# Performance work log

Measured on AMD Instinct MI355X. Metric: run time of the kernel, lower is better.

## Reference

```python
import jax, jax.numpy as jnp
import numpy as np

B, L, D = 4, 2048, 1024
H, DK, DV = 16, 64, 64


def setup_inputs() -> dict:
    key = jax.random.key(0)
    ks = jax.random.split(key, 11)
    s = 1.0 / np.sqrt(D)
    so = 1.0 / np.sqrt(H * DV)
    return {
        "query": jax.random.normal(ks[0], (B, L, D), jnp.float32),
        "key": jax.random.normal(ks[1], (B, L, D), jnp.float32),
        "value": jax.random.normal(ks[2], (B, L, D), jnp.float32),
        "W_q": jax.random.uniform(ks[3], (D, H * DK), jnp.float32, -s, s),
        "b_q": jax.random.uniform(ks[4], (H * DK,), jnp.float32, -s, s),
        "W_k": jax.random.uniform(ks[5], (D, H * DK), jnp.float32, -s, s),
        "b_k": jax.random.uniform(ks[6], (H * DK,), jnp.float32, -s, s),
        "W_v": jax.random.uniform(ks[7], (D, H * DV), jnp.float32, -s, s),
        "b_v": jax.random.uniform(ks[8], (H * DV,), jnp.float32, -s, s),
        "W_o": jax.random.uniform(ks[9], (H * DV, D), jnp.float32, -so, so),
        "b_o": jax.random.uniform(ks[10], (D,), jnp.float32, -so, so),
    }


def reference(query, key, value, W_q, b_q, W_k, b_k, W_v, b_v, W_o, b_o):
    # QKV projections, then split heads: [B, L, H*d] -> [B, H, L, d]
    q = (query @ W_q + b_q).reshape(B, L, H, DK).transpose(0, 2, 1, 3)
    k = (key @ W_k + b_k).reshape(B, L, H, DK).transpose(0, 2, 1, 3)
    v = (value @ W_v + b_v).reshape(B, L, H, DV).transpose(0, 2, 1, 3)
    # scaled dot-product attention: softmax(q k^T / sqrt(dk)) v
    scores = jnp.einsum("bhqd,bhkd->bhqk", q, k) / jnp.sqrt(jnp.float32(DK))
    attn = jax.nn.softmax(scores, axis=-1)
    ctx = jnp.einsum("bhqk,bhkd->bhqd", attn, v)
    # combine heads: [B, H, L, dv] -> [B, L, H*dv], output projection
    out = ctx.transpose(0, 2, 1, 3).reshape(B, L, H * DV) @ W_o + b_o
    return out
```

## Files before the change

kernel.cpp:

```cpp
#include <hip/hip_runtime.h>

#define BATCH 4
#define LSEQ 2048
#define DMODEL 1024
#define NHEAD 16
#define DHEAD 64
#define MTOT (BATCH * LSEQ)

typedef _Float16 f16;
typedef _Float16 f16x8 __attribute__((ext_vector_type(8)));
typedef _Float16 f16x4 __attribute__((ext_vector_type(4)));
typedef __fp16 h16x2 __attribute__((ext_vector_type(2)));
typedef float f32x4 __attribute__((ext_vector_type(4)));
typedef float f32x16 __attribute__((ext_vector_type(16)));
typedef unsigned int u32;
typedef unsigned int u32x4 __attribute__((ext_vector_type(4)));

#define SCORE_SCALE 0.180336878f

typedef const __attribute__((address_space(1))) void gvoid;
typedef __attribute__((address_space(3))) void lvoid;
#define GLDS16(g, l) __builtin_amdgcn_global_load_lds((gvoid*)(g), (lvoid*)(l), 16, 0, 0)

#define WAITCNT(s) do { asm volatile("s_waitcnt " s ::: "memory"); \
                        __builtin_amdgcn_sched_barrier(0); } while (0)
#define BAR() __builtin_amdgcn_s_barrier()
#define SCHED0() __builtin_amdgcn_sched_barrier(0)

__global__ __launch_bounds__(256)
void prep(const float* __restrict__ in0, const float* __restrict__ in1,
          const float* __restrict__ in2, f16* __restrict__ out, int n8,
          const float* __restrict__ W0, const float* __restrict__ W1,
          const float* __restrict__ W2, const float* __restrict__ W3,
          f16* __restrict__ WtBase)
{
    __shared__ float T[64][68];
    const int t = threadIdx.x;
    const int y = blockIdx.y;

    if (y < 3) {
        const float* in = (y == 0) ? in0 : (y == 1) ? in1 : in2;
        f16* o = out + (size_t)y * (size_t)n8 * 8;
        int i = blockIdx.x * 256 + t;
        if (i >= n8) return;
        float4 a = ((const float4*)in)[2 * i];
        float4 b = ((const float4*)in)[2 * i + 1];
        f16x8 v;
        v[0] = (f16)a.x; v[1] = (f16)a.y; v[2] = (f16)a.z; v[3] = (f16)a.w;
        v[4] = (f16)b.x; v[5] = (f16)b.y; v[6] = (f16)b.z; v[7] = (f16)b.w;
        ((f16x8*)o)[i] = v;
        return;
    }

    const int id = blockIdx.x;
    if (id >= 1024) return;
    const int z = id >> 8, rem = id & 255;
    const int k0 = (rem >> 4) * 64, n0 = (rem & 15) * 64;
    const float* W = (z == 0) ? W0 : (z == 1) ? W1 : (z == 2) ? W2 : W3;
    f16* Wt = WtBase + (size_t)z * DMODEL * DMODEL;
    const int tr = t >> 4, tc = (t & 15) * 4;
#pragma unroll
    for (int p = 0; p < 64; p += 16) {
        float4 v = *(const float4*)&W[(size_t)(k0 + tr + p) * DMODEL + n0 + tc];
        *(float4*)&T[tr + p][tc] = v;
    }
    __syncthreads();
    const int n = t >> 2, kc = (t & 3) * 16;
    f16x8 o0, o1;
#pragma unroll
    for (int j = 0; j < 8; ++j) o0[j] = (f16)T[kc + j][n];
#pragma unroll
    for (int j = 0; j < 8; ++j) o1[j] = (f16)T[kc + 8 + j][n];
    *(f16x8*)&Wt[(size_t)(n0 + n) * DMODEL + k0 + kc] = o0;
    *(f16x8*)&Wt[(size_t)(n0 + n) * DMODEL + k0 + kc + 8] = o1;
}

__global__ __launch_bounds__(512, 2)
void gemm_qkv(const f16* __restrict__ A, const f16* __restrict__ Bt,
              const float* __restrict__ b0, const float* __restrict__ b1,
              const float* __restrict__ b2, f16* __restrict__ Cout)
{
    __shared__ f16 As[2][2][128][64];
    __shared__ f16 Bs[2][2][128][64];

    const int t = threadIdx.x;
    const int lane = t & 63;
    const int w = t >> 6, wr = w >> 2, wc = w & 3;
    const int quad = lane >> 4, m16 = lane & 15;
    const int m0 = blockIdx.x * 256, n0 = blockIdx.y * 256;
    const int which = n0 >> 10;

    const int sr = t >> 3;
    const int sc = ((t & 7) << 4) ^ ((sr & 7) << 4);
    const f16* Asrc = A + (size_t)which * MTOT * DMODEL
                        + (size_t)(m0 + sr) * DMODEL + (sc >> 1);
    const f16* Bsrc = Bt + (size_t)(n0 + sr) * DMODEL + (sc >> 1);

    auto stA = [&](int buf, int h, int kt) {
        const f16* s = Asrc + (size_t)(h * 128) * DMODEL + kt * 64;
        GLDS16(s,               &As[buf][h][0][0] + t * 8);
        GLDS16(s + 64 * DMODEL, &As[buf][h][64][0] + t * 8);
    };
    auto stB = [&](int buf, int h, int kt) {
        const f16* s = Bsrc + (size_t)(h * 128) * DMODEL + kt * 64;
        GLDS16(s,               &Bs[buf][h][0][0] + t * 8);
        GLDS16(s + 64 * DMODEL, &Bs[buf][h][64][0] + t * 8);
    };
    auto stageTile = [&](int k) {
        const int b = k & 1;
        stA(b, 0, k); stA(b, 1, k); stB(b, 0, k); stB(b, 1, k);
    };

    const int fsw = (m16 & 7) << 4;
    auto rdA = [&](int buf, int mf, int ks) -> f16x8 {
        return *(const f16x8*)((const char*)&As[buf][wr][0][0]
                               + (mf * 16 + m16) * 128
                               + ((ks * 64 + quad * 16) ^ fsw));
    };
    auto rdB = [&](int buf, int nf, int ks) -> f16x8 {
        return *(const f16x8*)((const char*)&Bs[buf][wc >> 1][0][0]
                               + ((wc & 1) * 64 + nf * 16 + m16) * 128
                               + ((ks * 64 + quad * 16) ^ fsw));
    };

    f32x4 acc[8][4] = {};

    auto compute = [&](int buf) {
        f16x8 af[4][2], bf[4][2];
#pragma unroll
        for (int nf = 0; nf < 4; ++nf)
#pragma unroll
            for (int ks = 0; ks < 2; ++ks)
                bf[nf][ks] = rdB(buf, nf, ks);
#pragma unroll
        for (int mg = 0; mg < 2; ++mg) {
#pragma unroll
            for (int mi = 0; mi < 4; ++mi)
#pragma unroll
                for (int ks = 0; ks < 2; ++ks)
                    af[mi][ks] = rdA(buf, mg * 4 + mi, ks);
#pragma unroll
            for (int mi = 0; mi < 4; ++mi)
#pragma unroll
                for (int ni = 0; ni < 4; ++ni)
#pragma unroll
                    for (int ks = 0; ks < 2; ++ks)
                        acc[mg * 4 + mi][ni] =
                            __builtin_amdgcn_mfma_f32_16x16x32_f16(
                                af[mi][ks], bf[ni][ks],
                                acc[mg * 4 + mi][ni], 0, 0, 0);
        }
    };

    const int NKT = DMODEL / 64;
    stageTile(0);
    stageTile(1);

#pragma unroll 2
    for (int k = 0; k < NKT - 2; ++k) {
        WAITCNT("vmcnt(8)");
        BAR(); SCHED0();
        compute(k & 1);
        WAITCNT("lgkmcnt(0)");
        BAR(); SCHED0();
        stageTile(k + 2);
        SCHED0();
    }
    WAITCNT("vmcnt(8)");
    BAR(); SCHED0();
    compute((NKT - 2) & 1);
    WAITCNT("lgkmcnt(0)");
    BAR(); SCHED0();
    WAITCNT("vmcnt(0)");
    BAR(); SCHED0();
    compute((NKT - 1) & 1);

    const float* bp = (which == 0) ? b0 : (which == 1) ? b1 : b2;
    const float scale = (which == 0) ? SCORE_SCALE : 1.0f;
    f16* o = Cout + (size_t)which * MTOT * DMODEL;
    float bv[4];
    int hh[4], dd[4];
#pragma unroll
    for (int nf = 0; nf < 4; ++nf) {
        const int nn = (n0 + wc * 64 + nf * 16 + m16) & 1023;
        bv[nf] = bp[nn];
        hh[nf] = nn >> 6;
        dd[nf] = nn & 63;
    }
#pragma unroll
    for (int mf = 0; mf < 8; ++mf) {
        const int mrow = m0 + wr * 128 + mf * 16 + quad * 4;
        const int b = mrow >> 11, l0 = mrow & (LSEQ - 1);
        if (which < 2) {
#pragma unroll
            for (int j = 0; j < 4; ++j)
#pragma unroll
                for (int nf = 0; nf < 4; ++nf) {
                    const float v = (acc[mf][nf][j] + bv[nf]) * scale;
                    o[(((size_t)(b * NHEAD + hh[nf]) * LSEQ + l0 + j) << 6)
                      + dd[nf]] = (f16)v;
                }
        } else {
#pragma unroll
            for (int nf = 0; nf < 4; ++nf) {
                f16x4 pk;
#pragma unroll
                for (int j = 0; j < 4; ++j) pk[j] = (f16)(acc[mf][nf][j] + bv[nf]);
                *(f16x4*)&o[(((size_t)(b * NHEAD + hh[nf]) << 6) + dd[nf]) * LSEQ
                            + l0] = pk;
            }
        }
    }
}

__global__ __launch_bounds__(256)
void gemm_f16(const f16* __restrict__ A, const f16* __restrict__ Bt,
              const float* __restrict__ b0, void* __restrict__ Cout)
{
    __shared__ f16 As2[2][128][32];
    __shared__ f16 Bs2[2][128][32];

    const int t = threadIdx.x;
    const int lane = t & 63, w = t >> 6;
    const int quad = lane >> 4, m16 = lane & 15;
    const int m0 = blockIdx.x * 128;
    const int n0 = blockIdx.y * 128;
    const int wm = (w & 1) * 64, wn = (w >> 1) * 64;

    f32x4 acc[4][4] = {};

    const f16* Ag = A + (size_t)(m0 + (t >> 2)) * DMODEL + (t & 3) * 8;
    const f16* Bg = Bt + (size_t)(n0 + (t >> 2)) * DMODEL + (t & 3) * 8;
    f16* Al = &As2[0][0][0] + t * 8;
    f16* Bl = &Bs2[0][0][0] + t * 8;

    for (int k0 = 0; k0 < DMODEL; k0 += 64) {
        __syncthreads();
#pragma unroll
        for (int h = 0; h < 2; ++h) {
            GLDS16(Ag + k0 + h * 32, Al + h * 4096);
            GLDS16(Ag + k0 + h * 32 + (size_t)64 * DMODEL, Al + h * 4096 + 2048);
            GLDS16(Bg + k0 + h * 32, Bl + h * 4096);
            GLDS16(Bg + k0 + h * 32 + (size_t)64 * DMODEL, Bl + h * 4096 + 2048);
        }
        __syncthreads();
#pragma unroll
        for (int h = 0; h < 2; ++h) {
            f16x8 af[4], bf[4];
#pragma unroll
            for (int mi = 0; mi < 4; ++mi)
                af[mi] = *(const f16x8*)&As2[h][wm + mi * 16 + m16][quad * 8];
#pragma unroll
            for (int ni = 0; ni < 4; ++ni)
                bf[ni] = *(const f16x8*)&Bs2[h][wn + ni * 16 + m16][quad * 8];
#pragma unroll
            for (int mi = 0; mi < 4; ++mi)
#pragma unroll
                for (int ni = 0; ni < 4; ++ni)
                    acc[mi][ni] = __builtin_amdgcn_mfma_f32_16x16x32_f16(
                        af[mi], bf[ni], acc[mi][ni], 0, 0, 0);
        }
    }

#pragma unroll
    for (int ni = 0; ni < 4; ++ni) {
        const int n = n0 + wn + ni * 16 + m16;
        const float bv = b0[n];
#pragma unroll
        for (int mi = 0; mi < 4; ++mi)
#pragma unroll
            for (int j = 0; j < 4; ++j) {
                const int m = m0 + wm + mi * 16 + quad * 4 + j;
                ((float*)Cout)[(size_t)m * DMODEL + n] = acc[mi][ni][j] + bv;
            }
    }
}

__global__ __launch_bounds__(256, 4)
void attn_mfma(const f16* __restrict__ Qh, const f16* __restrict__ Kh,
               const f16* __restrict__ Vt, f16* __restrict__ ctx)
{
    __shared__ f16 Ks[2][64 * 64];
    __shared__ f16 Vs[2][64 * 64];

    const int t = threadIdx.x;
    const int lane = t & 63, w = t >> 6;
    const int l31 = lane & 31;
    const int hi = lane >> 5;
    const int swz = (l31 & 7) << 4;

    const int bid = blockIdx.x;
    const int x = bid & 7, rest = bid >> 3;
    const int qt = rest & 15;
    const int g = x + 8 * (rest >> 4);
    const int q0 = qt * 128 + w * 32;

    const f16* Qg = Qh + (size_t)g * LSEQ * DHEAD;
    const f16* Kg = Kh + (size_t)g * LSEQ * DHEAD;
    const f16* Vg = Vt + (size_t)g * LSEQ * DHEAD;

    f16x8 qf[4];
#pragma unroll
    for (int s = 0; s < 4; ++s)
        qf[s] = *(const f16x8*)&Qg[(size_t)(q0 + l31) * DHEAD + 16 * s + 8 * hi];

    const int srow = t >> 3;
    const int sxs = ((t & 7) << 4) ^ ((srow & 7) << 4);
    const f16* ksrcA = Kg + (size_t)srow * DHEAD + (sxs >> 1);
    const f16* vsrcA = Vg + (size_t)srow * LSEQ + (sxs >> 1);
    const f16* ksrcB = ksrcA + (size_t)32 * DHEAD;
    const f16* vsrcB = vsrcA + (size_t)32 * LSEQ;
    f16* kd[2] = {&Ks[0][0] + t * 8, &Ks[1][0] + t * 8};
    f16* vd[2] = {&Vs[0][0] + t * 8, &Vs[1][0] + t * 8};

    auto stage = [&](int b, int kt) {
        GLDS16(ksrcA + (size_t)kt * DHEAD, kd[b]);
        GLDS16(ksrcB + (size_t)kt * DHEAD, kd[b] + 2048);
        GLDS16(vsrcA + kt, vd[b]);
        GLDS16(vsrcB + kt, vd[b] + 2048);
    };

    f32x16 ctxa[2] = {};
    float lsum = 0.f;

    stage(0, 0);
    __syncthreads();

    auto proc = [&](const f32x16& stv, const int kb, const char* Vc) {
        u32 d[8];
        const h16x2 one2 = {(__fp16)1.0f, (__fp16)1.0f};
#pragma unroll
        for (int r = 0; r < 8; ++r) {
            const float p0 = __builtin_amdgcn_exp2f(stv[2 * r]);
            const float p1 = __builtin_amdgcn_exp2f(stv[2 * r + 1]);
            const h16x2 pk = __builtin_amdgcn_cvt_pkrtz(p0, p1);
#if __has_builtin(__builtin_amdgcn_fdot2)
            lsum = __builtin_amdgcn_fdot2(pk, one2, lsum, false);
#else
            lsum += p0 + p1;
#endif
            d[r] = __builtin_bit_cast(u32, pk);
        }
#pragma unroll
        for (int s = 0; s < 2; ++s) {
            const u32 sendE = hi ? d[4 * s + 0] : d[4 * s + 2];
            const u32 sendO = hi ? d[4 * s + 1] : d[4 * s + 3];
            const u32 recvE = __shfl_xor(sendE, 32);
            const u32 recvO = __shfl_xor(sendO, 32);
            u32x4 paw;
            paw[0] = hi ? recvE : d[4 * s + 0];
            paw[1] = hi ? recvO : d[4 * s + 1];
            paw[2] = hi ? d[4 * s + 2] : recvE;
            paw[3] = hi ? d[4 * s + 3] : recvO;
            const f16x8 pa = __builtin_bit_cast(f16x8, paw);
            const int kbyte = kb * 64 + 32 * s + 16 * hi;
#pragma unroll
            for (int d32 = 0; d32 < 2; ++d32) {
                const int vrow = d32 * 32 + l31;
                const f16x8 vf = *(const f16x8*)(Vc + vrow * 128 + (kbyte ^ swz));
                ctxa[d32] = __builtin_amdgcn_mfma_f32_32x32x16_f16(
                    pa, vf, ctxa[d32], 0, 0, 0);
            }
        }
    };

    auto compute = [&](const f16* Kbuf, const f16* Vbuf) {
        const char* Kc = (const char*)Kbuf;
        const char* Vc = (const char*)Vbuf;
        f32x16 s0 = {}, s1 = {};
#pragma unroll
        for (int s = 0; s < 4; ++s) {
            const int cb = 32 * s + 16 * hi;
            const f16x8 kf0 = *(const f16x8*)(Kc + l31 * 128 + (cb ^ swz));
            const f16x8 kf1 = *(const f16x8*)(Kc + (l31 + 32) * 128 + (cb ^ swz));
            s0 = __builtin_amdgcn_mfma_f32_32x32x16_f16(kf0, qf[s], s0, 0, 0, 0);
            s1 = __builtin_amdgcn_mfma_f32_32x32x16_f16(kf1, qf[s], s1, 0, 0, 0);
        }
        proc(s0, 0, Vc);
        proc(s1, 1, Vc);
    };

    for (int kt = 0; kt < LSEQ; kt += 128) {
        if (kt + 64 < LSEQ) stage(1, kt + 64);
        compute(&Ks[0][0], &Vs[0][0]);
        __syncthreads();
        if (kt + 128 < LSEQ) stage(0, kt + 128);
        compute(&Ks[1][0], &Vs[1][0]);
        __syncthreads();
    }

    const float l = lsum + __shfl_xor(lsum, 32);
    const float linv = 1.0f / l;
    const int batch = g >> 4, h = g & 15;
#pragma unroll
    for (int r = 0; r < 16; ++r) {
        const int qr = (r & 3) + 8 * (r >> 2) + 4 * hi;
        const float inv = __shfl(linv, qr);
        f16* op = ctx + ((size_t)(batch * LSEQ + q0 + qr)) * DMODEL
                      + h * 64 + l31;
        op[0]  = (f16)(ctxa[0][r] * inv);
        op[32] = (f16)(ctxa[1][r] * inv);
    }
}

extern "C" void kernel_launch(void* const* d_in, const int* in_sizes, int n_in,
                              void* d_out, int out_size, void* d_ws, size_t ws_size,
                              hipStream_t stream)
{
    const float* query = (const float*)d_in[0];
    const float* key   = (const float*)d_in[1];
    const float* value = (const float*)d_in[2];
    const float* W_q   = (const float*)d_in[3];
    const float* b_q   = (const float*)d_in[4];
    const float* W_k   = (const float*)d_in[5];
    const float* b_k   = (const float*)d_in[6];
    const float* W_v   = (const float*)d_in[7];
    const float* b_v   = (const float*)d_in[8];
    const float* W_o   = (const float*)d_in[9];
    const float* b_o   = (const float*)d_in[10];
    float* out = (float*)d_out;

    const size_t MAT = (size_t)MTOT * DMODEL;
    f16* base = (f16*)d_ws;
    f16* Aq   = base;
    f16* Qhp  = base + 3 * MAT;
    f16* ctxh = base + 6 * MAT;
    f16* Wtq  = base + 7 * MAT;
    f16* Wto  = Wtq + (size_t)3 * DMODEL * DMODEL;

    const int n8 = (int)(MAT / 8);
    prep<<<dim3(n8 / 256, 4), 256, 0, stream>>>(
        query, key, value, Aq, n8, W_q, W_k, W_v, W_o, Wtq);

    gemm_qkv<<<dim3(MTOT / 256, 3 * DMODEL / 256), 512, 0, stream>>>(
        Aq, Wtq, b_q, b_k, b_v, Qhp);

    attn_mfma<<<BATCH * NHEAD * (LSEQ / 128), 256, 0, stream>>>(
        Qhp, Qhp + MAT, Qhp + 2 * MAT, ctxh);

    gemm_f16<<<dim3(MTOT / 128, DMODEL / 128), 256, 0, stream>>>(
        ctxh, Wto, b_o, out);
}
```

Measured before the change: 342.0 us.

## Split attention KV tiles across wave pairs with 1024-thread blocks and LDS reduction

The attention kernel now runs 1024-thread blocks covering 256 query rows. Each pair of waves splits every 128-key tile between them, one taking the even half and one the odd half. The partial context sums and softmax denominators are then combined through shared memory. K/V staging moves to larger 128-key tiles with a wider V swizzle and explicit waitcnt/barrier pipelining, which amortizes K/V loads over more query rows. The trade-offs are an extra LDS reduction and larger blocks that may limit occupancy.

```diff
diff --git a/kernel.cpp b/kernel.cpp
--- a/kernel.cpp
+++ b/kernel.cpp
@@ -276,24 +276,26 @@
     }
 }
 
-__global__ __launch_bounds__(256, 4)
+__global__ __launch_bounds__(1024, 8)
 void attn_mfma(const f16* __restrict__ Qh, const f16* __restrict__ Kh,
                const f16* __restrict__ Vt, f16* __restrict__ ctx)
 {
-    __shared__ f16 Ks[2][64 * 64];
-    __shared__ f16 Vs[2][64 * 64];
+    __shared__ float SMf[16896];
+    char* smem = (char*)SMf;
 
     const int t = threadIdx.x;
     const int lane = t & 63, w = t >> 6;
+    const int qsub = w >> 1, par = w & 1;
     const int l31 = lane & 31;
     const int hi = lane >> 5;
-    const int swz = (l31 & 7) << 4;
+    const int swzK = (l31 & 7) << 4;
+    const int swzV = (l31 & 15) << 4;
 
     const int bid = blockIdx.x;
     const int x = bid & 7, rest = bid >> 3;
-    const int qt = rest & 15;
-    const int g = x + 8 * (rest >> 4);
-    const int q0 = qt * 128 + w * 32;
+    const int qt = rest & 7;
+    const int g = x + 8 * (rest >> 3);
+    const int q0 = qt * 256 + qsub * 32;
 
     const f16* Qg = Qh + (size_t)g * LSEQ * DHEAD;
     const f16* Kg = Kh + (size_t)g * LSEQ * DHEAD;
@@ -304,27 +306,20 @@
     for (int s = 0; s < 4; ++s)
         qf[s] = *(const f16x8*)&Qg[(size_t)(q0 + l31) * DHEAD + 16 * s + 8 * hi];
 
-    const int srow = t >> 3;
-    const int sxs = ((t & 7) << 4) ^ ((srow & 7) << 4);
-    const f16* ksrcA = Kg + (size_t)srow * DHEAD + (sxs >> 1);
-    const f16* vsrcA = Vg + (size_t)srow * LSEQ + (sxs >> 1);
-    const f16* ksrcB = ksrcA + (size_t)32 * DHEAD;
-    const f16* vsrcB = vsrcA + (size_t)32 * LSEQ;
-    f16* kd[2] = {&Ks[0][0] + t * 8, &Ks[1][0] + t * 8};
-    f16* vd[2] = {&Vs[0][0] + t * 8, &Vs[1][0] + t * 8};
-
-    auto stage = [&](int b, int kt) {
-        GLDS16(ksrcA + (size_t)kt * DHEAD, kd[b]);
-        GLDS16(ksrcB + (size_t)kt * DHEAD, kd[b] + 2048);
-        GLDS16(vsrcA + kt, vd[b]);
-        GLDS16(vsrcB + kt, vd[b] + 2048);
+    const int srK = t >> 3;
+    const int scK = ((t & 7) << 4) ^ ((srK & 7) << 4);
+    const f16* ksrc = Kg + (size_t)srK * DHEAD + (scK >> 1);
+    const int srV = t >> 4;
+    const int scV = ((t & 15) << 4) ^ ((srV & 15) << 4);
+    const f16* vsrc = Vg + (size_t)srV * LSEQ + (scV >> 1);
+
+    auto stage = [&](int b, int pr) {
+        GLDS16(ksrc + (size_t)(pr * 128) * DHEAD, (f16*)(smem + b * 16384) + t * 8);
+        GLDS16(vsrc + pr * 128, (f16*)(smem + 32768 + b * 16384) + t * 8);
     };
 
     f32x16 ctxa[2] = {};
     float lsum = 0.f;
-
-    stage(0, 0);
-    __syncthreads();
 
     auto proc = [&](const f32x16& stv, const int kb, const char* Vc) {
         u32 d[8];
@@ -353,26 +348,26 @@
             paw[2] = hi ? d[4 * s + 2] : recvE;
             paw[3] = hi ? d[4 * s + 3] : recvO;
             const f16x8 pa = __builtin_bit_cast(f16x8, paw);
-            const int kbyte = kb * 64 + 32 * s + 16 * hi;
+            const int kbyte = par * 128 + kb * 64 + 32 * s + 16 * hi;
 #pragma unroll
             for (int d32 = 0; d32 < 2; ++d32) {
                 const int vrow = d32 * 32 + l31;
-                const f16x8 vf = *(const f16x8*)(Vc + vrow * 128 + (kbyte ^ swz));
+                const f16x8 vf = *(const f16x8*)(Vc + vrow * 256 + (kbyte ^ swzV));
                 ctxa[d32] = __builtin_amdgcn_mfma_f32_32x32x16_f16(
                     pa, vf, ctxa[d32], 0, 0, 0);
             }
         }
     };
 
-    auto compute = [&](const f16* Kbuf, const f16* Vbuf) {
-        const char* Kc = (const char*)Kbuf;
-        const char* Vc = (const char*)Vbuf;
+    auto computeTile = [&](int b) {
+        const char* Kc = smem + b * 16384 + par * 8192;
+        const char* Vc = smem + 32768 + b * 16384;
         f32x16 s0 = {}, s1 = {};
 #pragma unroll
         for (int s = 0; s < 4; ++s) {
             const int cb = 32 * s + 16 * hi;
-            const f16x8 kf0 = *(const f16x8*)(Kc + l31 * 128 + (cb ^ swz));
-            const f16x8 kf1 = *(const f16x8*)(Kc + (l31 + 32) * 128 + (cb ^ swz));
+            const f16x8 kf0 = *(const f16x8*)(Kc + l31 * 128 + (cb ^ swzK));
+            const f16x8 kf1 = *(const f16x8*)(Kc + (l31 + 32) * 128 + (cb ^ swzK));
             s0 = __builtin_amdgcn_mfma_f32_32x32x16_f16(kf0, qf[s], s0, 0, 0, 0);
             s1 = __builtin_amdgcn_mfma_f32_32x32x16_f16(kf1, qf[s], s1, 0, 0, 0);
         }
@@ -380,26 +375,56 @@
         proc(s1, 1, Vc);
     };
 
-    for (int kt = 0; kt < LSEQ; kt += 128) {
-        if (kt + 64 < LSEQ) stage(1, kt + 64);
-        compute(&Ks[0][0], &Vs[0][0]);
-        __syncthreads();
-        if (kt + 128 < LSEQ) stage(0, kt + 128);
-        compute(&Ks[1][0], &Vs[1][0]);
-        __syncthreads();
-    }
-
-    const float l = lsum + __shfl_xor(lsum, 32);
-    const float linv = 1.0f / l;
-    const int batch = g >> 4, h = g & 15;
-#pragma unroll
-    for (int r = 0; r < 16; ++r) {
-        const int qr = (r & 3) + 8 * (r >> 2) + 4 * hi;
-        const float inv = __shfl(linv, qr);
-        f16* op = ctx + ((size_t)(batch * LSEQ + q0 + qr)) * DMODEL
-                      + h * 64 + l31;
-        op[0]  = (f16)(ctxa[0][r] * inv);
-        op[32] = (f16)(ctxa[1][r] * inv);
+    stage(0, 0);
+    stage(1, 1);
+
+#pragma unroll 2
+    for (int i = 0; i < 14; ++i) {
+        WAITCNT("vmcnt(2)");
+        BAR(); SCHED0();
+        computeTile(i & 1);
+        WAITCNT("lgkmcnt(0)");
+        BAR(); SCHED0();
+        stage(i & 1, i + 2);
+        SCHED0();
+    }
+    WAITCNT("vmcnt(2)");
+    BAR(); SCHED0();
+    computeTile(0);
+    WAITCNT("lgkmcnt(0)");
+    BAR(); SCHED0();
+    WAITCNT("vmcnt(0)");
+    computeTile(1);
+
+    __syncthreads();
+    const float lw = lsum + __shfl_xor(lsum, 32);
+    const int slot = (qsub * 64 + lane) * 33;
+    if (par) {
+#pragma unroll
+        for (int r = 0; r < 16; ++r) {
+            SMf[slot + r]      = ctxa[0][r];
+            SMf[slot + 16 + r] = ctxa[1][r];
+        }
+        SMf[slot + 32] = lw;
+    }
+    __syncthreads();
+    if (!par) {
+#pragma unroll
+        for (int r = 0; r < 16; ++r) {
+            ctxa[0][r] += SMf[slot + r];
+            ctxa[1][r] += SMf[slot + 16 + r];
+        }
+        const float linv = 1.0f / (lw + SMf[slot + 32]);
+        const int batch = g >> 4, h = g & 15;
+#pragma unroll
+        for (int r = 0; r < 16; ++r) {
+            const int qr = (r & 3) + 8 * (r >> 2) + 4 * hi;
+            const float inv = __shfl(linv, qr);
+            f16* op = ctx + ((size_t)(batch * LSEQ + q0 + qr)) * DMODEL
+                          + h * 64 + l31;
+            op[0]  = (f16)(ctxa[0][r] * inv);
+            op[32] = (f16)(ctxa[1][r] * inv);
+        }
     }
 }
 
@@ -435,7 +460,7 @@
     gemm_qkv<<<dim3(MTOT / 256, 3 * DMODEL / 256), 512, 0, stream>>>(
         Aq, Wtq, b_q, b_k, b_v, Qhp);
 
-    attn_mfma<<<BATCH * NHEAD * (LSEQ / 128), 256, 0, stream>>>(
+    attn_mfma<<<BATCH * NHEAD * (LSEQ / 256), 1024, 0, stream>>>(
         Qhp, Qhp + MAT, Qhp + 2 * MAT, ctxh);
 
     gemm_f16<<<dim3(MTOT / 128, DMODEL / 128), 256, 0, stream>>>(
```

Measured after the change: 869.8 us. 154% more time.
